# Optimization experiments

Hardware: AMD Instinct MI355X
Metric: run time of the kernel (lower is better)

Reference implementation:

```python
import jax, jax.numpy as jnp
import numpy as np

B, L, D, H = 4, 1024, 512, 8
HEAD_DIM = D // H
WINDOW = 32
HALF = WINDOW // 2
TEMP = 1.0
PAT_TEMP = 0.3
THRESHOLD = 0.05
SPARSITY = 0.3


def setup_inputs() -> dict:
    key = jax.random.key(0)
    ks = jax.random.split(key, 12)
    s = 0.02
    x = jax.random.normal(ks[0], (B, L, D), jnp.float32)
    qkv_w = jax.random.normal(ks[1], (3 * D, D), jnp.float32) * s
    proj_w = jax.random.normal(ks[2], (D, D), jnp.float32) * s
    proj_b = jnp.zeros((D,), jnp.float32)
    ps_w1 = jax.random.normal(ks[3], (D, D), jnp.float32) * s
    ps_b1 = jnp.zeros((D,), jnp.float32)
    ps_w2 = jax.random.normal(ks[4], (D // 2, D), jnp.float32) * s
    ps_b2 = jnp.zeros((D // 2,), jnp.float32)
    ps_w3 = jax.random.normal(ks[5], (3, D // 2), jnp.float32) * 0.1
    ps_b3 = jnp.array([1.0, -0.5, -0.5], jnp.float32)
    pattern_bias = jnp.array([0.2, -0.1, -0.1], jnp.float32)
    sparse_w = jax.random.normal(ks[6], (H,), jnp.float32) * 0.3
    sparse_b = jnp.zeros((H,), jnp.float32)
    return dict(x=x, qkv_w=qkv_w, proj_w=proj_w, proj_b=proj_b,
                ps_w1=ps_w1, ps_b1=ps_b1, ps_w2=ps_w2, ps_b2=ps_b2,
                ps_w3=ps_w3, ps_b3=ps_b3, pattern_bias=pattern_bias,
                sparse_w=sparse_w, sparse_b=sparse_b)


def _forward(x, qkv_w, proj_w, proj_b, ps_w1, ps_b1, ps_w2, ps_b2,
             ps_w3, ps_b3, pattern_bias, sparse_w, sparse_b):
    b, l, d = x.shape
    scale = HEAD_DIM ** -0.5
    # QKV projection and head split -> (B, H, L, head_dim)
    qkv = (x @ qkv_w.T).reshape(b, l, 3, H, HEAD_DIM)
    qkv = jnp.transpose(qkv, (2, 0, 3, 1, 4))
    q, k, v = qkv[0], qkv[1], qkv[2]
    scores = jnp.einsum('bhqd,bhkd->bhqk', q, k) * scale  # (B,H,L,L)

    # Pattern selector on mean-pooled features
    pooled = x.mean(axis=1)
    h1 = jax.nn.relu(pooled @ ps_w1.T + ps_b1)
    h2 = jax.nn.relu(h1 @ ps_w2.T + ps_b2)
    logits = h2 @ ps_w3.T + ps_b3 + pattern_bias  # (B, 3)
    pw = jax.nn.softmax(logits / PAT_TEMP, axis=-1)

    # Local window mask (L, L): |i - j| <= half
    idx = jnp.arange(l)
    local_mask = (jnp.abs(idx[:, None] - idx[None, :]) <= HALF).astype(jnp.float32)

    # Learned sparse mask via per-head affine + topk scatter
    s2 = scores * sparse_w[None, :, None, None] + sparse_b[None, :, None, None]
    k_top = max(1, min(l, int(l * (1.0 - SPARSITY))))
    _, ti = jax.lax.top_k(s2, k_top)  # (B,H,L,k)
    flat_idx = ti.reshape(-1, k_top)
    rows = jnp.arange(flat_idx.shape[0])[:, None]
    sparse_mask = jnp.zeros((b * H * l, l), jnp.float32).at[rows, flat_idx].set(1.0)
    sparse_mask = sparse_mask.reshape(b, H, l, l)

    # Blend masks per-sample (global mask is all ones)
    combined = (pw[:, 0, None, None, None] * local_mask
                + pw[:, 1, None, None, None]
                + pw[:, 2, None, None, None] * sparse_mask)
    allow = combined > THRESHOLD
    masked = jnp.where(allow, scores, -jnp.inf)

    # If a row is fully masked, unmask position 0 with score 0.0
    all_masked = ~allow.any(axis=-1)  # (B,H,L)
    masked = masked.at[..., 0].set(jnp.where(all_masked, 0.0, masked[..., 0]))

    attn = jax.nn.softmax(masked / TEMP, axis=-1)
    out = jnp.einsum('bhqk,bhkd->bhqd', attn, v)
    out = jnp.transpose(out, (0, 2, 1, 3)).reshape(b, l, d)
    return out @ proj_w.T + proj_b


def reference(x, qkv_w, proj_w, proj_b, ps_w1, ps_b1, ps_w2, ps_b2,
              ps_w3, ps_b3, pattern_bias, sparse_w, sparse_b):
    return _forward(x, qkv_w, proj_w, proj_b, ps_w1, ps_b1, ps_w2, ps_b2,
                    ps_w3, ps_b3, pattern_bias, sparse_w, sparse_b)
```

## Files before the change

kernel.cpp:

```cpp
#include <hip/hip_runtime.h>
#include <hip/hip_bf16.h>
#include <math.h>

#define NB 4
#define SEQ 1024
#define DIM 512
#define NH 8
#define HDIM 64
#define HALFW 16
#define KTOP 716
#define THRESH 0.05f
#define PATT 0.3f
#define SCALE 0.125f
#define QKVN 1536

typedef __attribute__((ext_vector_type(8))) short bf16x8;
typedef __attribute__((ext_vector_type(4))) float f32x4;

__device__ __forceinline__ void async_load16(const void* g, void* l) {
  __builtin_amdgcn_global_load_lds(
      (const __attribute__((address_space(1))) void*)g,
      (__attribute__((address_space(3))) void*)l, 16, 0, 0);
}

__device__ __forceinline__ void cvt8(const float* s, __hip_bfloat16* d) {
  float4 a = *(const float4*)s;
  float4 b = *(const float4*)(s + 4);
  union { __hip_bfloat16 h[8]; uint4 u; } o;
  o.h[0] = __float2bfloat16(a.x); o.h[1] = __float2bfloat16(a.y);
  o.h[2] = __float2bfloat16(a.z); o.h[3] = __float2bfloat16(a.w);
  o.h[4] = __float2bfloat16(b.x); o.h[5] = __float2bfloat16(b.y);
  o.h[6] = __float2bfloat16(b.z); o.h[7] = __float2bfloat16(b.w);
  *(uint4*)d = o.u;
}

__device__ __forceinline__ bf16x8 pack8_scalar(const float* p) {
  union { __hip_bfloat16 h[8]; bf16x8 v; } o;
#pragma unroll
  for (int i = 0; i < 8; ++i) o.h[i] = __float2bfloat16(p[i]);
  return o.v;
}
__device__ __forceinline__ bf16x8 pack8_vec(const float* p) {
  float4 a = *(const float4*)p;
  float4 b = *(const float4*)(p + 4);
  union { __hip_bfloat16 h[8]; bf16x8 v; } o;
  o.h[0] = __float2bfloat16(a.x); o.h[1] = __float2bfloat16(a.y);
  o.h[2] = __float2bfloat16(a.z); o.h[3] = __float2bfloat16(a.w);
  o.h[4] = __float2bfloat16(b.x); o.h[5] = __float2bfloat16(b.y);
  o.h[6] = __float2bfloat16(b.z); o.h[7] = __float2bfloat16(b.w);
  return o.v;
}

__device__ __forceinline__ float wave_sum(float v) {
#pragma unroll
  for (int m = 32; m >= 1; m >>= 1) v += __shfl_xor(v, m);
  return v;
}

__global__ __launch_bounds__(256) void cvt_pool_kernel(
    const float* __restrict__ x, const float* __restrict__ wq,
    const float* __restrict__ wp,
    __hip_bfloat16* __restrict__ xb, __hip_bfloat16* __restrict__ wqb,
    __hip_bfloat16* __restrict__ wpb, float* __restrict__ partial) {
  int bid = blockIdx.x, t = threadIdx.x;
  if (bid < 128) {
    int b = bid >> 5, c = bid & 31;
    size_t base = ((size_t)b * SEQ + (size_t)c * 32) * DIM;
    int g = t & 63;
    int r0 = t >> 6;
    float s[8] = {};
    for (int rr = r0; rr < 32; rr += 4) {
      const float* src = x + base + (size_t)rr * DIM + g * 8;
      float4 a = *(const float4*)src;
      float4 bq = *(const float4*)(src + 4);
      union { __hip_bfloat16 h[8]; uint4 u; } o;
      o.h[0] = __float2bfloat16(a.x); o.h[1] = __float2bfloat16(a.y);
      o.h[2] = __float2bfloat16(a.z); o.h[3] = __float2bfloat16(a.w);
      o.h[4] = __float2bfloat16(bq.x); o.h[5] = __float2bfloat16(bq.y);
      o.h[6] = __float2bfloat16(bq.z); o.h[7] = __float2bfloat16(bq.w);
      *(uint4*)(xb + base + (size_t)rr * DIM + g * 8) = o.u;
      s[0] += a.x; s[1] += a.y; s[2] += a.z; s[3] += a.w;
      s[4] += bq.x; s[5] += bq.y; s[6] += bq.z; s[7] += bq.w;
    }
    __shared__ float red[4][DIM];
#pragma unroll
    for (int u = 0; u < 8; ++u) red[r0][g * 8 + u] = s[u];
    __syncthreads();
    for (int d = t; d < DIM; d += 256)
      partial[(size_t)bid * DIM + d] = red[0][d] + red[1][d] + red[2][d] + red[3][d];
  } else {
    int wi = bid - 128;
#pragma unroll
    for (int u = 0; u < 4; ++u) {
      int gidx = wi * 1024 + u * 256 + t;
      if (gidx < 98304) cvt8(wq + (size_t)gidx * 8, wqb + (size_t)gidx * 8);
      else { int j = gidx - 98304; cvt8(wp + (size_t)j * 8, wpb + (size_t)j * 8); }
    }
  }
}

__global__ __launch_bounds__(256) void qkv_mlp1_kernel(
    const __hip_bfloat16* __restrict__ A, const __hip_bfloat16* __restrict__ B,
    float* __restrict__ C, int N, int K,
    const float* __restrict__ partial, const float* __restrict__ w1,
    const float* __restrict__ b1, float* __restrict__ h1) {
  __shared__ __hip_bfloat16 As[128 * 32];
  __shared__ __hip_bfloat16 Bs[64 * 32];
  __shared__ float pooled[DIM];
  int t = threadIdx.x;
  int bid = blockIdx.x;
  if (bid < 768) {
    int ntiles = N >> 6;
    int m0 = (bid / ntiles) * 128;
    int n0 = (bid % ntiles) * 64;
    int w = t >> 6, l = t & 63;
    int fm = l & 15, fg = l >> 4;
    f32x4 acc[2][4] = {};
    for (int k0 = 0; k0 < K; k0 += 32) {
#pragma unroll
      for (int i = 0; i < 2; ++i) {
        int s = i * 256 + t;
        int row = s >> 2, cb = (s & 3) << 4;
        async_load16((const char*)(A + (size_t)(m0 + row) * K + k0) + cb,
                     (char*)As + (size_t)s * 16);
      }
      {
        int row = t >> 2, cb = (t & 3) << 4;
        async_load16((const char*)(B + (size_t)(n0 + row) * K + k0) + cb,
                     (char*)Bs + (size_t)t * 16);
      }
      __syncthreads();
      bf16x8 af[2], bf[4];
#pragma unroll
      for (int i = 0; i < 2; ++i)
        af[i] = *(const bf16x8*)(As + (size_t)(w * 32 + i * 16 + fm) * 32 + fg * 8);
#pragma unroll
      for (int j = 0; j < 4; ++j)
        bf[j] = *(const bf16x8*)(Bs + (size_t)(j * 16 + fm) * 32 + fg * 8);
#pragma unroll
      for (int i = 0; i < 2; ++i)
#pragma unroll
        for (int j = 0; j < 4; ++j)
          acc[i][j] = __builtin_amdgcn_mfma_f32_16x16x32_bf16(af[i], bf[j], acc[i][j], 0, 0, 0);
      __syncthreads();
    }
#pragma unroll
    for (int i = 0; i < 2; ++i) {
      int mbase = m0 + w * 32 + i * 16 + fg * 4;
#pragma unroll
      for (int j = 0; j < 4; ++j) {
        int n = n0 + j * 16 + fm;
#pragma unroll
        for (int r = 0; r < 4; ++r)
          C[(size_t)(mbase + r) * N + n] = acc[i][j][r];
      }
    }
  } else {
    int idx = bid - 768;
    int b = idx >> 7;
    int i0 = (idx & 127) << 2;
    for (int d = t; d < DIM; d += 256) {
      float acc = 0.f;
#pragma unroll 8
      for (int c = 0; c < 32; ++c) acc += partial[(size_t)(b * 32 + c) * DIM + d];
      pooled[d] = acc * (1.0f / SEQ);
    }
    __syncthreads();
    int wv = t >> 6, lane = t & 63;
    int i = i0 + wv;
    const float* w = w1 + (size_t)i * DIM + lane * 8;
    float4 p0 = *(const float4*)(pooled + lane * 8);
    float4 p1 = *(const float4*)(pooled + lane * 8 + 4);
    float4 w0 = *(const float4*)w;
    float4 wx = *(const float4*)(w + 4);
    float acc = fmaf(p0.x, w0.x, fmaf(p0.y, w0.y, fmaf(p0.z, w0.z, p0.w * w0.w)));
    acc = fmaf(p1.x, wx.x, fmaf(p1.y, wx.y, fmaf(p1.z, wx.z, fmaf(p1.w, wx.w, acc))));
    acc = wave_sum(acc);
    if (lane == 0) h1[b * DIM + i] = fmaxf(acc + b1[i], 0.f);
  }
}

__global__ __launch_bounds__(256) void mlp2_kernel(
    const float* __restrict__ h1, const float* __restrict__ w2,
    const float* __restrict__ b2, float* __restrict__ h2) {
  int gw = blockIdx.x * 4 + (threadIdx.x >> 6);
  int lane = threadIdx.x & 63;
  int b = gw >> 8, i = gw & 255;
  const float* p = h1 + (size_t)b * DIM + lane * 8;
  const float* w = w2 + (size_t)i * DIM + lane * 8;
  float4 p0 = *(const float4*)p;
  float4 p1 = *(const float4*)(p + 4);
  float4 w0 = *(const float4*)w;
  float4 wv = *(const float4*)(w + 4);
  float acc = fmaf(p0.x, w0.x, fmaf(p0.y, w0.y, fmaf(p0.z, w0.z, p0.w * w0.w)));
  acc = fmaf(p1.x, wv.x, fmaf(p1.y, wv.y, fmaf(p1.z, wv.z, fmaf(p1.w, wv.w, acc))));
  acc = wave_sum(acc);
  if (lane == 0) h2[gw] = fmaxf(acc + b2[i], 0.f);
}

__global__ __launch_bounds__(64) void mlp3_flags_kernel(
    const float* __restrict__ h2, const float* __restrict__ w3,
    const float* __restrict__ b3, const float* __restrict__ pbias,
    float* __restrict__ flags) {
  int b = blockIdx.x;
  int lane = threadIdx.x;
  const float* h = h2 + (size_t)b * (DIM / 2) + lane * 4;
  float4 hv = *(const float4*)h;
  float lg[3];
#pragma unroll
  for (int o = 0; o < 3; ++o) {
    const float* w = w3 + (size_t)o * (DIM / 2) + lane * 4;
    float4 wv = *(const float4*)w;
    float acc = fmaf(hv.x, wv.x, fmaf(hv.y, wv.y, fmaf(hv.z, wv.z, hv.w * wv.w)));
    acc = wave_sum(acc);
    lg[o] = (acc + b3[o] + pbias[o]) * (1.0f / PATT);
  }
  if (lane == 0) {
    float m = fmaxf(lg[0], fmaxf(lg[1], lg[2]));
    float e0 = expf(lg[0] - m), e1 = expf(lg[1] - m), e2 = expf(lg[2] - m);
    float s = e0 + e1 + e2;
    float p0 = e0 / s, p1 = e1 / s, p2 = e2 / s;
    float* f = flags + b * 16;
    f[0] = p0; f[1] = p1; f[2] = p2;
    float cn = (p1 > THRESH) ? 1.f : 0.f;
    float cl = (p0 + p1 > THRESH) ? 1.f : 0.f;
    float cs = (p1 + p2 > THRESH) ? 1.f : 0.f;
    float cls = (p0 + p1 + p2 > THRESH) ? 1.f : 0.f;
    f[3] = cn; f[4] = cl; f[5] = cs; f[6] = cls;
    f[7] = ((cls != cl) || (cs != cn)) ? 1.f : 0.f;
  }
}

__device__ __forceinline__ int block_sum_i(int v, int* red, int t) {
#pragma unroll
  for (int m = 32; m >= 1; m >>= 1) v += __shfl_xor(v, m);
  __syncthreads();
  if ((t & 63) == 0) red[t >> 6] = v;
  __syncthreads();
  return red[0] + red[1] + red[2] + red[3];
}
__device__ __forceinline__ float block_sum_f(float v, float* red, int t) {
#pragma unroll
  for (int m = 32; m >= 1; m >>= 1) v += __shfl_xor(v, m);
  __syncthreads();
  if ((t & 63) == 0) red[t >> 6] = v;
  __syncthreads();
  return red[0] + red[1] + red[2] + red[3];
}
__device__ __forceinline__ float block_max_f(float v, float* red, int t) {
#pragma unroll
  for (int m = 32; m >= 1; m >>= 1) v = fmaxf(v, __shfl_xor(v, m));
  __syncthreads();
  if ((t & 63) == 0) red[t >> 6] = v;
  __syncthreads();
  return fmaxf(fmaxf(red[0], red[1]), fmaxf(red[2], red[3]));
}

union AttnSmem {
  struct { float Ks[96][65]; float Vt[64][116]; short Px[4][16][72]; } band;
  struct { float s[SEQ]; float q[HDIM]; unsigned u[SEQ]; int a[SEQ]; int b2[SEQ];
           float rf[4]; int ri[4]; } gen;
};

__global__ __launch_bounds__(256) void attn_kernel(
    const float* __restrict__ flags, const float* __restrict__ qkv,
    const float* __restrict__ sw, const float* __restrict__ sb,
    __hip_bfloat16* __restrict__ ao) {
  __shared__ AttnSmem sm;
  int t = threadIdx.x;
  if (blockIdx.x < 512) {
    int bid = blockIdx.x;
    int q64 = bid & 15;
    int h = (bid >> 4) & 7;
    int b = bid >> 7;
    const float* f = flags + b * 16;
    if (f[7] > 0.5f || f[3] > 0.5f) return;
    const float* base = qkv + (size_t)b * SEQ * QKVN;
    int ho = h * HDIM;
    int q0 = q64 << 6;

    if (f[4] < 0.5f) {
      int d = t & 63;
      float val = base[1024 + ho + d];
      for (int qq = t >> 6; qq < 64; qq += 4)
        ao[((size_t)b * SEQ + q0 + qq) * DIM + ho + d] = __float2bfloat16(val);
      return;
    }

    int w = t >> 6, l = t & 63;
    int fm = l & 15, fg = l >> 4;
    int j0 = q0 - 16;

    for (int token = t; token < 112 * 16; token += 256) {
      int row = token >> 4, seg = token & 15;
      int jg = j0 + row;
      bool ok = (row < 96) && (jg >= 0) && (jg < SEQ);
      float4 kv = make_float4(0.f, 0.f, 0.f, 0.f);
      float4 vv = make_float4(0.f, 0.f, 0.f, 0.f);
      if (ok) {
        const float* src = base + (size_t)jg * QKVN + 512 + ho + seg * 4;
        kv = *(const float4*)src;
        vv = *(const float4*)(src + 512);
      }
      if (row < 96) {
        float* kd = &sm.band.Ks[row][seg * 4];
        kd[0] = kv.x; kd[1] = kv.y; kd[2] = kv.z; kd[3] = kv.w;
      }
      int d0 = seg * 4;
      sm.band.Vt[d0 + 0][row] = vv.x;
      sm.band.Vt[d0 + 1][row] = vv.y;
      sm.band.Vt[d0 + 2][row] = vv.z;
      sm.band.Vt[d0 + 3][row] = vv.w;
    }
    {
      int r = l >> 2, cg = (l & 3) << 2;
      *(uint2*)&sm.band.Px[w][r][48 + cg] = make_uint2(0u, 0u);
    }
    bf16x8 aq[2];
    {
      int qrow = q0 + w * 16 + fm;
      const float* qsrc = base + (size_t)qrow * QKVN + ho;
#pragma unroll
      for (int c = 0; c < 2; ++c) aq[c] = pack8_vec(qsrc + c * 32 + fg * 8);
    }
    __syncthreads();

    f32x4 sacc[3] = {};
#pragma unroll
    for (int jt = 0; jt < 3; ++jt)
#pragma unroll
      for (int c = 0; c < 2; ++c) {
        bf16x8 bk = pack8_scalar(&sm.band.Ks[w * 16 + jt * 16 + fm][c * 32 + fg * 8]);
        sacc[jt] = __builtin_amdgcn_mfma_f32_16x16x32_bf16(aq[c], bk, sacc[jt], 0, 0, 0);
      }
    float pv[3][4];
#pragma unroll
    for (int r = 0; r < 4; ++r) {
      int ql = fg * 4 + r;
      float sv[3], mx = -INFINITY;
#pragma unroll
      for (int jt = 0; jt < 3; ++jt) {
        int jl = jt * 16 + fm;
        int jg = j0 + w * 16 + jl;
        int d = jl - ql;
        bool valid = (d >= 0) && (d <= 32) && (jg >= 0) && (jg < SEQ);
        sv[jt] = valid ? sacc[jt][r] * SCALE : -INFINITY;
        mx = fmaxf(mx, sv[jt]);
      }
#pragma unroll
      for (int msk = 8; msk >= 1; msk >>= 1) mx = fmaxf(mx, __shfl_xor(mx, msk));
      float sum = 0.f;
#pragma unroll
      for (int jt = 0; jt < 3; ++jt) {
        float p = (sv[jt] == -INFINITY) ? 0.f : expf(sv[jt] - mx);
        pv[jt][r] = p; sum += p;
      }
#pragma unroll
      for (int msk = 8; msk >= 1; msk >>= 1) sum += __shfl_xor(sum, msk);
      float inv = 1.f / sum;
#pragma unroll
      for (int jt = 0; jt < 3; ++jt) {
        union { __hip_bfloat16 hh; short ss; } cv;
        cv.hh = __float2bfloat16(pv[jt][r] * inv);
        sm.band.Px[w][ql][jt * 16 + fm] = cv.ss;
      }
    }
    bf16x8 pa[2];
#pragma unroll
    for (int c = 0; c < 2; ++c)
      pa[c] = *(const bf16x8*)&sm.band.Px[w][fm][c * 32 + fg * 8];
    f32x4 oacc[4] = {};
#pragma unroll
    for (int dt = 0; dt < 4; ++dt)
#pragma unroll
      for (int c = 0; c < 2; ++c) {
        bf16x8 bv = pack8_vec(&sm.band.Vt[dt * 16 + fm][w * 16 + c * 32 + fg * 8]);
        oacc[dt] = __builtin_amdgcn_mfma_f32_16x16x32_bf16(pa[c], bv, oacc[dt], 0, 0, 0);
      }
#pragma unroll
    for (int dt = 0; dt < 4; ++dt)
#pragma unroll
      for (int r = 0; r < 4; ++r) {
        int qg = q0 + w * 16 + fg * 4 + r;
        ao[((size_t)b * SEQ + qg) * DIM + ho + dt * 16 + fm] =
            __float2bfloat16(oacc[dt][r]);
      }
  } else {
    int bid = blockIdx.x - 512;
    int qg = bid & 255;
    int h = (bid >> 8) & 7;
    int b = bid >> 11;
    const float* f = flags + b * 16;
    bool need_sparse = f[7] > 0.5f;
    bool cn_b = f[3] > 0.5f;
    if (!(need_sparse || cn_b)) return;

    const float* base = qkv + (size_t)b * SEQ * QKVN;
    int ho = h * HDIM;
    float c_n = f[3], c_l = f[4], c_s = f[5], c_ls = f[6];
    float swh = sw[h], sbh = sb[h];

    float* s_sh = sm.gen.s;
    float* q_sh = sm.gen.q;
    unsigned* u_sh = sm.gen.u;
    int* sc_a = sm.gen.a;
    int* sc_b = sm.gen.b2;
    float* redf = sm.gen.rf;
    int* redi = sm.gen.ri;

    for (int qi = 0; qi < 4; ++qi) {
      int q = qg * 4 + qi;
      if (t < HDIM) q_sh[t] = base[(size_t)q * QKVN + ho + t];
      __syncthreads();
      for (int j = t; j < SEQ; j += 256) {
        const float* kr = base + (size_t)j * QKVN + 512 + ho;
        float acc = 0.f;
#pragma unroll
        for (int dd = 0; dd < HDIM; ++dd) acc = fmaf(q_sh[dd], kr[dd], acc);
        s_sh[j] = acc * SCALE;
      }
      __syncthreads();

      if (need_sparse) {
        for (int j = t; j < SEQ; j += 256) {
          unsigned bits = __float_as_uint(fmaf(s_sh[j], swh, sbh));
          u_sh[j] = bits ^ ((bits & 0x80000000u) ? 0xFFFFFFFFu : 0x80000000u);
        }
        __syncthreads();
        unsigned V = 0u;
        for (int bit = 31; bit >= 0; --bit) {
          unsigned cand = V | (1u << bit);
          int c = 0;
          for (int j = t; j < SEQ; j += 256) c += (u_sh[j] >= cand) ? 1 : 0;
          c = block_sum_i(c, redi, t);
          if (c >= KTOP) V = cand;
        }
        int g = 0;
        for (int j = t; j < SEQ; j += 256) g += (u_sh[j] > V) ? 1 : 0;
        g = block_sum_i(g, redi, t);
        int r = KTOP - g;
        for (int j = t; j < SEQ; j += 256) sc_a[j] = (u_sh[j] == V) ? 1 : 0;
        __syncthreads();
        int* src = sc_a; int* dst = sc_b;
        for (int off = 1; off < SEQ; off <<= 1) {
          for (int j = t; j < SEQ; j += 256)
            dst[j] = src[j] + ((j >= off) ? src[j - off] : 0);
          __syncthreads();
          int* tmp = src; src = dst; dst = tmp;
        }
        for (int j = t; j < SEQ; j += 256) {
          bool sp = (u_sh[j] > V) || ((u_sh[j] == V) && (src[j] - 1 < r));
          bool local = (j >= q - HALFW) && (j <= q + HALFW);
          float cv = local ? (sp ? c_ls : c_l) : (sp ? c_s : c_n);
          if (cv < 0.5f) s_sh[j] = -INFINITY;
        }
      } else {
        for (int j = t; j < SEQ; j += 256) {
          bool local = (j >= q - HALFW) && (j <= q + HALFW);
          float cv = local ? c_l : c_n;
          if (cv < 0.5f) s_sh[j] = -INFINITY;
        }
      }
      __syncthreads();

      int anyc = 0;
      for (int j = t; j < SEQ; j += 256) anyc += (s_sh[j] != -INFINITY) ? 1 : 0;
      anyc = block_sum_i(anyc, redi, t);
      if (anyc == 0 && t == 0) s_sh[0] = 0.f;
      __syncthreads();

      float mx = -INFINITY;
      for (int j = t; j < SEQ; j += 256) mx = fmaxf(mx, s_sh[j]);
      mx = block_max_f(mx, redf, t);
      float ls = 0.f;
      for (int j = t; j < SEQ; j += 256) {
        float p = (s_sh[j] == -INFINITY) ? 0.f : expf(s_sh[j] - mx);
        s_sh[j] = p; ls += p;
      }
      ls = block_sum_f(ls, redf, t);
      float inv = 1.f / ls;

      int dd = t & 63, jg = t >> 6;
      float acc = 0.f;
      for (int j = jg; j < SEQ; j += 4)
        acc = fmaf(s_sh[j] * inv, base[(size_t)j * QKVN + 1024 + ho + dd], acc);
      float* redo = (float*)u_sh;
      __syncthreads();
      redo[t] = acc;
      __syncthreads();
      if (t < 64) {
        float o = redo[t] + redo[t + 64] + redo[t + 128] + redo[t + 192];
        ao[((size_t)b * SEQ + q) * DIM + ho + t] = __float2bfloat16(o);
      }
      __syncthreads();
    }
  }
}

__global__ __launch_bounds__(256) void proj_gemm_kernel(
    const __hip_bfloat16* __restrict__ A, const __hip_bfloat16* __restrict__ B,
    const float* __restrict__ bias, float* __restrict__ C,
    int N, int K) {
  __shared__ __hip_bfloat16 As[128 * 32];
  __shared__ __hip_bfloat16 Bs[64 * 32];
  int t = threadIdx.x;
  int m0 = blockIdx.y * 128;
  int n0 = blockIdx.x * 64;
  int w = t >> 6, l = t & 63;
  int fm = l & 15, fg = l >> 4;
  f32x4 acc[2][4] = {};
  for (int k0 = 0; k0 < K; k0 += 32) {
#pragma unroll
    for (int i = 0; i < 2; ++i) {
      int s = i * 256 + t;
      int row = s >> 2, cb = (s & 3) << 4;
      async_load16((const char*)(A + (size_t)(m0 + row) * K + k0) + cb,
                   (char*)As + (size_t)s * 16);
    }
    {
      int row = t >> 2, cb = (t & 3) << 4;
      async_load16((const char*)(B + (size_t)(n0 + row) * K + k0) + cb,
                   (char*)Bs + (size_t)t * 16);
    }
    __syncthreads();
    bf16x8 af[2], bf[4];
#pragma unroll
    for (int i = 0; i < 2; ++i)
      af[i] = *(const bf16x8*)(As + (size_t)(w * 32 + i * 16 + fm) * 32 + fg * 8);
#pragma unroll
    for (int j = 0; j < 4; ++j)
      bf[j] = *(const bf16x8*)(Bs + (size_t)(j * 16 + fm) * 32 + fg * 8);
#pragma unroll
    for (int i = 0; i < 2; ++i)
#pragma unroll
      for (int j = 0; j < 4; ++j)
        acc[i][j] = __builtin_amdgcn_mfma_f32_16x16x32_bf16(af[i], bf[j], acc[i][j], 0, 0, 0);
    __syncthreads();
  }
#pragma unroll
  for (int i = 0; i < 2; ++i) {
    int mbase = m0 + w * 32 + i * 16 + fg * 4;
#pragma unroll
    for (int j = 0; j < 4; ++j) {
      int n = n0 + j * 16 + fm;
      float bv = bias[n];
#pragma unroll
      for (int r = 0; r < 4; ++r)
        C[(size_t)(mbase + r) * N + n] = acc[i][j][r] + bv;
    }
  }
}

extern "C" void kernel_launch(void* const* d_in, const int* in_sizes, int n_in,
                              void* d_out, int out_size, void* d_ws, size_t ws_size,
                              hipStream_t stream) {
  const float* x      = (const float*)d_in[0];
  const float* qkv_w  = (const float*)d_in[1];
  const float* proj_w = (const float*)d_in[2];
  const float* proj_b = (const float*)d_in[3];
  const float* ps_w1  = (const float*)d_in[4];
  const float* ps_b1  = (const float*)d_in[5];
  const float* ps_w2  = (const float*)d_in[6];
  const float* ps_b2  = (const float*)d_in[7];
  const float* ps_w3  = (const float*)d_in[8];
  const float* ps_b3  = (const float*)d_in[9];
  const float* pbias  = (const float*)d_in[10];
  const float* sw     = (const float*)d_in[11];
  const float* sb     = (const float*)d_in[12];
  float* out = (float*)d_out;

  char* w = (char*)d_ws;
  float* flags = (float*)w;              w += 256;
  float* partial = (float*)w;            w += (size_t)NB * 32 * DIM * 4;
  float* h1 = (float*)w;                 w += (size_t)NB * DIM * 4;
  float* h2 = (float*)w;                 w += (size_t)NB * (DIM / 2) * 4;
  float* qkv = (float*)w;                w += (size_t)NB * SEQ * QKVN * 4;
  __hip_bfloat16* xb  = (__hip_bfloat16*)w;  w += (size_t)NB * SEQ * DIM * 2;
  __hip_bfloat16* wqb = (__hip_bfloat16*)w;  w += (size_t)QKVN * DIM * 2;
  __hip_bfloat16* wpb = (__hip_bfloat16*)w;  w += (size_t)DIM * DIM * 2;
  __hip_bfloat16* aob = (__hip_bfloat16*)w;  w += (size_t)NB * SEQ * DIM * 2;

  hipLaunchKernelGGL(cvt_pool_kernel, dim3(256), dim3(256), 0, stream,
                     x, qkv_w, proj_w, xb, wqb, wpb, partial);
  hipLaunchKernelGGL(qkv_mlp1_kernel, dim3(768 + 512), dim3(256), 0, stream,
                     xb, wqb, qkv, QKVN, DIM, partial, ps_w1, ps_b1, h1);
  hipLaunchKernelGGL(mlp2_kernel, dim3(256), dim3(256), 0, stream,
                     h1, ps_w2, ps_b2, h2);
  hipLaunchKernelGGL(mlp3_flags_kernel, dim3(NB), dim3(64), 0, stream,
                     h2, ps_w3, ps_b3, pbias, flags);
  hipLaunchKernelGGL(attn_kernel, dim3(512 + 8192), dim3(256), 0, stream,
                     flags, qkv, sw, sb, aob);
  hipLaunchKernelGGL(proj_gemm_kernel, dim3(DIM / 64, (NB * SEQ) / 128), dim3(256), 0, stream,
                     aob, wpb, proj_b, out, DIM, DIM);
}
```

Baseline: 132.8 us.

## Store QKV in bf16 and fold pattern-selector softmax into attention kernel

The QKV GEMM now writes bf16 instead of fp32. Attention reads bf16 K/V/Q directly into LDS with vector loads, so the per-fragment fp32-to-bf16 packing disappears. The tiny mlp3_flags kernel is removed and every attention block recomputes the 3-way pattern softmax and flags into shared memory, saving one launch. This halves QKV traffic but adds redundant per-block MLP work and lowers the precision of the fallback dense path's scores.

```diff
diff --git a/kernel.cpp b/kernel.cpp
--- a/kernel.cpp
+++ b/kernel.cpp
@@ -34,21 +34,8 @@
   *(uint4*)d = o.u;
 }
 
-__device__ __forceinline__ bf16x8 pack8_scalar(const float* p) {
-  union { __hip_bfloat16 h[8]; bf16x8 v; } o;
-#pragma unroll
-  for (int i = 0; i < 8; ++i) o.h[i] = __float2bfloat16(p[i]);
-  return o.v;
-}
-__device__ __forceinline__ bf16x8 pack8_vec(const float* p) {
-  float4 a = *(const float4*)p;
-  float4 b = *(const float4*)(p + 4);
-  union { __hip_bfloat16 h[8]; bf16x8 v; } o;
-  o.h[0] = __float2bfloat16(a.x); o.h[1] = __float2bfloat16(a.y);
-  o.h[2] = __float2bfloat16(a.z); o.h[3] = __float2bfloat16(a.w);
-  o.h[4] = __float2bfloat16(b.x); o.h[5] = __float2bfloat16(b.y);
-  o.h[6] = __float2bfloat16(b.z); o.h[7] = __float2bfloat16(b.w);
-  return o.v;
+__device__ __forceinline__ float b2f(short v) {
+  return __uint_as_float(((unsigned)(unsigned short)v) << 16);
 }
 
 __device__ __forceinline__ float wave_sum(float v) {
@@ -101,7 +88,7 @@
 
 __global__ __launch_bounds__(256) void qkv_mlp1_kernel(
     const __hip_bfloat16* __restrict__ A, const __hip_bfloat16* __restrict__ B,
-    float* __restrict__ C, int N, int K,
+    __hip_bfloat16* __restrict__ C, int N, int K,
     const float* __restrict__ partial, const float* __restrict__ w1,
     const float* __restrict__ b1, float* __restrict__ h1) {
   __shared__ __hip_bfloat16 As[128 * 32];
@@ -152,7 +139,7 @@
         int n = n0 + j * 16 + fm;
 #pragma unroll
         for (int r = 0; r < 4; ++r)
-          C[(size_t)(mbase + r) * N + n] = acc[i][j][r];
+          C[(size_t)(mbase + r) * N + n] = __float2bfloat16(acc[i][j][r]);
       }
     }
   } else {
@@ -198,39 +185,6 @@
   if (lane == 0) h2[gw] = fmaxf(acc + b2[i], 0.f);
 }
 
-__global__ __launch_bounds__(64) void mlp3_flags_kernel(
-    const float* __restrict__ h2, const float* __restrict__ w3,
-    const float* __restrict__ b3, const float* __restrict__ pbias,
-    float* __restrict__ flags) {
-  int b = blockIdx.x;
-  int lane = threadIdx.x;
-  const float* h = h2 + (size_t)b * (DIM / 2) + lane * 4;
-  float4 hv = *(const float4*)h;
-  float lg[3];
-#pragma unroll
-  for (int o = 0; o < 3; ++o) {
-    const float* w = w3 + (size_t)o * (DIM / 2) + lane * 4;
-    float4 wv = *(const float4*)w;
-    float acc = fmaf(hv.x, wv.x, fmaf(hv.y, wv.y, fmaf(hv.z, wv.z, hv.w * wv.w)));
-    acc = wave_sum(acc);
-    lg[o] = (acc + b3[o] + pbias[o]) * (1.0f / PATT);
-  }
-  if (lane == 0) {
-    float m = fmaxf(lg[0], fmaxf(lg[1], lg[2]));
-    float e0 = expf(lg[0] - m), e1 = expf(lg[1] - m), e2 = expf(lg[2] - m);
-    float s = e0 + e1 + e2;
-    float p0 = e0 / s, p1 = e1 / s, p2 = e2 / s;
-    float* f = flags + b * 16;
-    f[0] = p0; f[1] = p1; f[2] = p2;
-    float cn = (p1 > THRESH) ? 1.f : 0.f;
-    float cl = (p0 + p1 > THRESH) ? 1.f : 0.f;
-    float cs = (p1 + p2 > THRESH) ? 1.f : 0.f;
-    float cls = (p0 + p1 + p2 > THRESH) ? 1.f : 0.f;
-    f[3] = cn; f[4] = cl; f[5] = cs; f[6] = cls;
-    f[7] = ((cls != cl) || (cs != cn)) ? 1.f : 0.f;
-  }
-}
-
 __device__ __forceinline__ int block_sum_i(int v, int* red, int t) {
 #pragma unroll
   for (int m = 32; m >= 1; m >>= 1) v += __shfl_xor(v, m);
@@ -257,33 +211,65 @@
 }
 
 union AttnSmem {
-  struct { float Ks[96][65]; float Vt[64][116]; short Px[4][16][72]; } band;
+  struct { short Ks[96][72]; short Vt[64][120]; short Px[4][16][72]; } band;
   struct { float s[SEQ]; float q[HDIM]; unsigned u[SEQ]; int a[SEQ]; int b2[SEQ];
            float rf[4]; int ri[4]; } gen;
 };
 
 __global__ __launch_bounds__(256) void attn_kernel(
-    const float* __restrict__ flags, const float* __restrict__ qkv,
+    const float* __restrict__ h2, const float* __restrict__ w3,
+    const float* __restrict__ b3, const float* __restrict__ pbias,
+    const __hip_bfloat16* __restrict__ qkvb,
     const float* __restrict__ sw, const float* __restrict__ sb,
     __hip_bfloat16* __restrict__ ao) {
   __shared__ AttnSmem sm;
+  __shared__ float fl[8];
   int t = threadIdx.x;
-  if (blockIdx.x < 512) {
-    int bid = blockIdx.x;
+  bool banded = blockIdx.x < 512;
+  int bid = banded ? blockIdx.x : blockIdx.x - 512;
+  int b = banded ? (bid >> 7) : (bid >> 11);
+
+  if (t < 64) {
+    float4 hv = *(const float4*)(h2 + (size_t)b * (DIM / 2) + t * 4);
+    float lg[3];
+#pragma unroll
+    for (int o = 0; o < 3; ++o) {
+      const float* w = w3 + (size_t)o * (DIM / 2) + t * 4;
+      float4 wv = *(const float4*)w;
+      float acc = fmaf(hv.x, wv.x, fmaf(hv.y, wv.y, fmaf(hv.z, wv.z, hv.w * wv.w)));
+      acc = wave_sum(acc);
+      lg[o] = (acc + b3[o] + pbias[o]) * (1.0f / PATT);
+    }
+    if (t == 0) {
+      float m = fmaxf(lg[0], fmaxf(lg[1], lg[2]));
+      float e0 = expf(lg[0] - m), e1 = expf(lg[1] - m), e2 = expf(lg[2] - m);
+      float s = e0 + e1 + e2;
+      float p0 = e0 / s, p1 = e1 / s, p2 = e2 / s;
+      fl[0] = p0; fl[1] = p1; fl[2] = p2;
+      float cn = (p1 > THRESH) ? 1.f : 0.f;
+      float cl = (p0 + p1 > THRESH) ? 1.f : 0.f;
+      float cs = (p1 + p2 > THRESH) ? 1.f : 0.f;
+      float cls = (p0 + p1 + p2 > THRESH) ? 1.f : 0.f;
+      fl[3] = cn; fl[4] = cl; fl[5] = cs; fl[6] = cls;
+      fl[7] = ((cls != cl) || (cs != cn)) ? 1.f : 0.f;
+    }
+  }
+  __syncthreads();
+
+  const short* base = (const short*)qkvb + (size_t)b * SEQ * QKVN;
+
+  if (banded) {
     int q64 = bid & 15;
     int h = (bid >> 4) & 7;
-    int b = bid >> 7;
-    const float* f = flags + b * 16;
-    if (f[7] > 0.5f || f[3] > 0.5f) return;
-    const float* base = qkv + (size_t)b * SEQ * QKVN;
+    if (fl[7] > 0.5f || fl[3] > 0.5f) return;
     int ho = h * HDIM;
     int q0 = q64 << 6;
 
-    if (f[4] < 0.5f) {
+    if (fl[4] < 0.5f) {
       int d = t & 63;
-      float val = base[1024 + ho + d];
+      short val = base[1024 + ho + d];
       for (int qq = t >> 6; qq < 64; qq += 4)
-        ao[((size_t)b * SEQ + q0 + qq) * DIM + ho + d] = __float2bfloat16(val);
+        *((short*)ao + ((size_t)b * SEQ + q0 + qq) * DIM + ho + d) = val;
       return;
     }
 
@@ -291,26 +277,26 @@
     int fm = l & 15, fg = l >> 4;
     int j0 = q0 - 16;
 
-    for (int token = t; token < 112 * 16; token += 256) {
-      int row = token >> 4, seg = token & 15;
+    for (int tt = t; tt < 768; tt += 256) {
+      int row = tt >> 3, seg = tt & 7;
       int jg = j0 + row;
-      bool ok = (row < 96) && (jg >= 0) && (jg < SEQ);
-      float4 kv = make_float4(0.f, 0.f, 0.f, 0.f);
-      float4 vv = make_float4(0.f, 0.f, 0.f, 0.f);
-      if (ok) {
-        const float* src = base + (size_t)jg * QKVN + 512 + ho + seg * 4;
-        kv = *(const float4*)src;
-        vv = *(const float4*)(src + 512);
-      }
-      if (row < 96) {
-        float* kd = &sm.band.Ks[row][seg * 4];
-        kd[0] = kv.x; kd[1] = kv.y; kd[2] = kv.z; kd[3] = kv.w;
-      }
-      int d0 = seg * 4;
-      sm.band.Vt[d0 + 0][row] = vv.x;
-      sm.band.Vt[d0 + 1][row] = vv.y;
-      sm.band.Vt[d0 + 2][row] = vv.z;
-      sm.band.Vt[d0 + 3][row] = vv.w;
+      jg = jg < 0 ? 0 : (jg > SEQ - 1 ? SEQ - 1 : jg);
+      bf16x8 kv = *(const bf16x8*)(base + (size_t)jg * QKVN + 512 + ho + seg * 8);
+      *(bf16x8*)&sm.band.Ks[row][seg * 8] = kv;
+    }
+    for (int tt = t; tt < 768; tt += 256) {
+      int row = tt % 96, seg = tt / 96;
+      int jg = j0 + row;
+      jg = jg < 0 ? 0 : (jg > SEQ - 1 ? SEQ - 1 : jg);
+      union { bf16x8 v; short s[8]; } vv;
+      vv.v = *(const bf16x8*)(base + (size_t)jg * QKVN + 1024 + ho + seg * 8);
+      int d0 = seg * 8;
+#pragma unroll
+      for (int i = 0; i < 8; ++i) sm.band.Vt[d0 + i][row] = vv.s[i];
+    }
+    {
+      int r = t >> 2, cg = (t & 3) << 2;
+      *(uint2*)&sm.band.Vt[r][96 + cg] = make_uint2(0u, 0u);
     }
     {
       int r = l >> 2, cg = (l & 3) << 2;
@@ -319,9 +305,9 @@
     bf16x8 aq[2];
     {
       int qrow = q0 + w * 16 + fm;
-      const float* qsrc = base + (size_t)qrow * QKVN + ho;
-#pragma unroll
-      for (int c = 0; c < 2; ++c) aq[c] = pack8_vec(qsrc + c * 32 + fg * 8);
+      const short* qsrc = base + (size_t)qrow * QKVN + ho;
+#pragma unroll
+      for (int c = 0; c < 2; ++c) aq[c] = *(const bf16x8*)(qsrc + c * 32 + fg * 8);
     }
     __syncthreads();
 
@@ -330,10 +316,9 @@
     for (int jt = 0; jt < 3; ++jt)
 #pragma unroll
       for (int c = 0; c < 2; ++c) {
-        bf16x8 bk = pack8_scalar(&sm.band.Ks[w * 16 + jt * 16 + fm][c * 32 + fg * 8]);
+        bf16x8 bk = *(const bf16x8*)&sm.band.Ks[w * 16 + jt * 16 + fm][c * 32 + fg * 8];
         sacc[jt] = __builtin_amdgcn_mfma_f32_16x16x32_bf16(aq[c], bk, sacc[jt], 0, 0, 0);
       }
-    float pv[3][4];
 #pragma unroll
     for (int r = 0; r < 4; ++r) {
       int ql = fg * 4 + r;
@@ -349,11 +334,11 @@
       }
 #pragma unroll
       for (int msk = 8; msk >= 1; msk >>= 1) mx = fmaxf(mx, __shfl_xor(mx, msk));
-      float sum = 0.f;
+      float pv[3], sum = 0.f;
 #pragma unroll
       for (int jt = 0; jt < 3; ++jt) {
         float p = (sv[jt] == -INFINITY) ? 0.f : expf(sv[jt] - mx);
-        pv[jt][r] = p; sum += p;
+        pv[jt] = p; sum += p;
       }
 #pragma unroll
       for (int msk = 8; msk >= 1; msk >>= 1) sum += __shfl_xor(sum, msk);
@@ -361,7 +346,7 @@
 #pragma unroll
       for (int jt = 0; jt < 3; ++jt) {
         union { __hip_bfloat16 hh; short ss; } cv;
-        cv.hh = __float2bfloat16(pv[jt][r] * inv);
+        cv.hh = __float2bfloat16(pv[jt] * inv);
         sm.band.Px[w][ql][jt * 16 + fm] = cv.ss;
       }
     }
@@ -374,7 +359,7 @@
     for (int dt = 0; dt < 4; ++dt)
 #pragma unroll
       for (int c = 0; c < 2; ++c) {
-        bf16x8 bv = pack8_vec(&sm.band.Vt[dt * 16 + fm][w * 16 + c * 32 + fg * 8]);
+        bf16x8 bv = *(const bf16x8*)&sm.band.Vt[dt * 16 + fm][w * 16 + c * 32 + fg * 8];
         oacc[dt] = __builtin_amdgcn_mfma_f32_16x16x32_bf16(pa[c], bv, oacc[dt], 0, 0, 0);
       }
 #pragma unroll
@@ -386,18 +371,14 @@
             __float2bfloat16(oacc[dt][r]);
       }
   } else {
-    int bid = blockIdx.x - 512;
     int qg = bid & 255;
     int h = (bid >> 8) & 7;
-    int b = bid >> 11;
-    const float* f = flags + b * 16;
-    bool need_sparse = f[7] > 0.5f;
-    bool cn_b = f[3] > 0.5f;
+    bool need_sparse = fl[7] > 0.5f;
+    bool cn_b = fl[3] > 0.5f;
     if (!(need_sparse || cn_b)) return;
 
-    const float* base = qkv + (size_t)b * SEQ * QKVN;
     int ho = h * HDIM;
-    float c_n = f[3], c_l = f[4], c_s = f[5], c_ls = f[6];
+    float c_n = fl[3], c_l = fl[4], c_s = fl[5], c_ls = fl[6];
     float swh = sw[h], sbh = sb[h];
 
     float* s_sh = sm.gen.s;
@@ -410,13 +391,19 @@
 
     for (int qi = 0; qi < 4; ++qi) {
       int q = qg * 4 + qi;
-      if (t < HDIM) q_sh[t] = base[(size_t)q * QKVN + ho + t];
+      if (t < HDIM) q_sh[t] = b2f(base[(size_t)q * QKVN + ho + t]);
       __syncthreads();
       for (int j = t; j < SEQ; j += 256) {
-        const float* kr = base + (size_t)j * QKVN + 512 + ho;
+        const short* kr = base + (size_t)j * QKVN + 512 + ho;
         float acc = 0.f;
 #pragma unroll
-        for (int dd = 0; dd < HDIM; ++dd) acc = fmaf(q_sh[dd], kr[dd], acc);
+        for (int c = 0; c < 8; ++c) {
+          union { bf16x8 v; short s[8]; } kv;
+          kv.v = *(const bf16x8*)(kr + c * 8);
+#pragma unroll
+          for (int i = 0; i < 8; ++i)
+            acc = fmaf(q_sh[c * 8 + i], b2f(kv.s[i]), acc);
+        }
         s_sh[j] = acc * SCALE;
       }
       __syncthreads();
@@ -480,10 +467,10 @@
       ls = block_sum_f(ls, redf, t);
       float inv = 1.f / ls;
 
-      int dd = t & 63, jg = t >> 6;
+      int dd = t & 63, jg2 = t >> 6;
       float acc = 0.f;
-      for (int j = jg; j < SEQ; j += 4)
-        acc = fmaf(s_sh[j] * inv, base[(size_t)j * QKVN + 1024 + ho + dd], acc);
+      for (int j = jg2; j < SEQ; j += 4)
+        acc = fmaf(s_sh[j] * inv, b2f(base[(size_t)j * QKVN + 1024 + ho + dd]), acc);
       float* redo = (float*)u_sh;
       __syncthreads();
       redo[t] = acc;
@@ -570,11 +557,10 @@
   float* out = (float*)d_out;
 
   char* w = (char*)d_ws;
-  float* flags = (float*)w;              w += 256;
   float* partial = (float*)w;            w += (size_t)NB * 32 * DIM * 4;
   float* h1 = (float*)w;                 w += (size_t)NB * DIM * 4;
   float* h2 = (float*)w;                 w += (size_t)NB * (DIM / 2) * 4;
-  float* qkv = (float*)w;                w += (size_t)NB * SEQ * QKVN * 4;
+  __hip_bfloat16* qkvb = (__hip_bfloat16*)w; w += (size_t)NB * SEQ * QKVN * 2;
   __hip_bfloat16* xb  = (__hip_bfloat16*)w;  w += (size_t)NB * SEQ * DIM * 2;
   __hip_bfloat16* wqb = (__hip_bfloat16*)w;  w += (size_t)QKVN * DIM * 2;
   __hip_bfloat16* wpb = (__hip_bfloat16*)w;  w += (size_t)DIM * DIM * 2;
@@ -583,13 +569,11 @@
   hipLaunchKernelGGL(cvt_pool_kernel, dim3(256), dim3(256), 0, stream,
                      x, qkv_w, proj_w, xb, wqb, wpb, partial);
   hipLaunchKernelGGL(qkv_mlp1_kernel, dim3(768 + 512), dim3(256), 0, stream,
-                     xb, wqb, qkv, QKVN, DIM, partial, ps_w1, ps_b1, h1);
+                     xb, wqb, qkvb, QKVN, DIM, partial, ps_w1, ps_b1, h1);
   hipLaunchKernelGGL(mlp2_kernel, dim3(256), dim3(256), 0, stream,
                      h1, ps_w2, ps_b2, h2);
-  hipLaunchKernelGGL(mlp3_flags_kernel, dim3(NB), dim3(64), 0, stream,
-                     h2, ps_w3, ps_b3, pbias, flags);
   hipLaunchKernelGGL(attn_kernel, dim3(512 + 8192), dim3(256), 0, stream,
-                     flags, qkv, sw, sb, aob);
+                     h2, ps_w3, ps_b3, pbias, qkvb, sw, sb, aob);
   hipLaunchKernelGGL(proj_gemm_kernel, dim3(DIM / 64, (NB * SEQ) / 128), dim3(256), 0, stream,
                      aob, wpb, proj_b, out, DIM, DIM);
 }
```

Result: no change. 132.2 us (-0.5%).
